# Performance work log

Hardware: AMD Instinct MI355X
Metric: run time of the kernel (lower is better)

## Reference

```python
import jax, jax.numpy as jnp
import numpy as np

KSIZE = 7       # patch size
STRIDE_Q = 4    # stride_1: query patch stride
STRIDE_KV = 1   # stride_2: key/value patch stride
SCALE = 10.0    # softmax_scale


def unfold(x, k, stride, pad):
    """torch.nn.Unfold equivalent. x:[B,C,H,W] -> [B, C*k*k, L] (c-major, then kh, kw)."""
    x = jnp.pad(x, ((0, 0), (0, 0), (pad, pad), (pad, pad)))
    B, C, Hp, Wp = x.shape
    nh = (Hp - k) // stride + 1
    nw = (Wp - k) // stride + 1
    sl = lambda i, n: slice(i, i + (n - 1) * stride + 1, stride)
    # [B, C, k*k, nh, nw]
    pat = jnp.stack([x[:, :, sl(i, nh), sl(j, nw)] for i in range(k) for j in range(k)], axis=2)
    return pat.reshape(B, C * k * k, nh * nw)


def fold(p, k, stride, pad, H, W):
    """torch.nn.functional.fold equivalent (overlap-add). p:[B, C*k*k, L] -> [B,C,H,W]."""
    B, D, L = p.shape
    C = D // (k * k)
    nh = (H + 2 * pad - k) // stride + 1
    nw = (W + 2 * pad - k) // stride + 1
    p = p.reshape(B, C, k, k, nh, nw)
    out = jnp.zeros((B, C, H + 2 * pad, W + 2 * pad), p.dtype)
    sl = lambda i, n: slice(i, i + (n - 1) * stride + 1, stride)
    for i in range(k):
        for j in range(k):
            out = out.at[:, :, sl(i, nh), sl(j, nw)].add(p[:, :, i, j])
    return out[:, :, pad:pad + H, pad:pad + W]


def conv1x1(x, w, bias):
    # w: [out, in]
    return jnp.einsum('bihw,oi->bohw', x, w) + bias[None, :, None, None]


def setup_inputs() -> dict:
    key = jax.random.key(0)
    ks = jax.random.split(key, 9)
    B, Cin, H, W = 4, 64, 128, 128
    Cit = 16
    s_in = 1.0 / np.sqrt(Cin)
    s_it = 1.0 / np.sqrt(Cit)
    return {
        'b': jax.random.normal(ks[0], (B, Cin, H, W), jnp.float32),
        'g_w': jax.random.normal(ks[1], (Cit, Cin), jnp.float32) * s_in,
        'g_b': jax.random.normal(ks[2], (Cit,), jnp.float32) * 0.01,
        'th_w': jax.random.normal(ks[3], (Cit, Cin), jnp.float32) * s_in,
        'th_b': jax.random.normal(ks[4], (Cit,), jnp.float32) * 0.01,
        'ph_w': jax.random.normal(ks[5], (Cit, Cin), jnp.float32) * s_in,
        'ph_b': jax.random.normal(ks[6], (Cit,), jnp.float32) * 0.01,
        'o_w': jax.random.normal(ks[7], (Cin, Cit), jnp.float32) * s_it,
        'o_b': jax.random.normal(ks[8], (Cin,), jnp.float32) * 0.01,
    }


def reference(b, g_w, g_b, th_w, th_b, ph_w, ph_b, o_w, o_b):
    B, Cin, H, W = b.shape
    pad = KSIZE // 2
    b1 = conv1x1(b, g_w, g_b)      # queries source  [B,16,H,W]
    b2 = conv1x1(b, th_w, th_b)    # values source
    b3 = conv1x1(b, ph_w, ph_b)    # keys source

    Q = unfold(b1, KSIZE, STRIDE_Q, pad).transpose(0, 2, 1)   # [B, L1, D]
    K = unfold(b3, KSIZE, STRIDE_KV, pad).transpose(0, 2, 1)  # [B, L2, D]
    V = unfold(b2, KSIZE, STRIDE_KV, pad).transpose(0, 2, 1)  # [B, L2, D]

    scores = jnp.einsum('bqd,bkd->bqk', Q, K)                 # [B, L1, L2]
    attn = jax.nn.softmax(scores * SCALE, axis=-1)
    Zp = jnp.einsum('bqk,bkd->bqd', attn, V).transpose(0, 2, 1)  # [B, D, L1]

    y = fold(Zp, KSIZE, STRIDE_Q, pad, H, W)                  # overlap-add
    Zc = fold(jnp.ones_like(Zp), KSIZE, STRIDE_Q, pad, H, W)  # overlap counts
    y = y / Zc
    y = conv1x1(y, o_w, o_b)
    return b + y
```

## Files before the change

kernel.cpp:

```cpp
#include <hip/hip_runtime.h>
#include <math.h>

#define NB 4
#define CIN 64
#define CIT 16
#define KS 7
#define PAD 3
#define HH 128
#define WW 128
#define HP 134
#define WPS 136
#define L1 1024
#define DD 784
#define SCALE_F 10.0f
#define WSCR 3.5f
#define TCAP 128
#define WEPS 1e-7f

#define NPIX (HP * WPS)
#define NHWCF (NB * NPIX * CIT)
#define RSTR 2176

typedef __attribute__((ext_vector_type(4))) float f32x4;
typedef __attribute__((ext_vector_type(8))) short s16x8;
typedef __attribute__((ext_vector_type(4))) unsigned int u32x4;

__device__ __forceinline__ unsigned short f2bf(float f) {
    unsigned u = __float_as_uint(f);
    unsigned r = (u + 0x7FFFu + ((u >> 16) & 1u)) >> 16;
    return (unsigned short)r;
}

__global__ __launch_bounds__(256) void k_prep(
    const float* __restrict__ bin,
    const float* __restrict__ gw, const float* __restrict__ gb,
    const float* __restrict__ tw, const float* __restrict__ tb,
    const float* __restrict__ pw, const float* __restrict__ pb,
    float* __restrict__ b1f, float* __restrict__ b2f, float* __restrict__ b3f,
    unsigned short* __restrict__ b1n, unsigned short* __restrict__ b3n)
{
    int p = blockIdx.x * 256 + threadIdx.x;
    if (p >= NB * NPIX) return;
    int x = p % WPS; int r = p / WPS; int y = r % HP; int bb = r / HP;
    bool inter = (x >= PAD && x < PAD + WW && y >= PAD && y < PAD + HH);
    float v[CIN];
    if (inter) {
        int iy = y - PAD, ix = x - PAD;
        const float* src = bin + ((size_t)(bb * CIN) * HH + iy) * WW + ix;
        #pragma unroll
        for (int ci = 0; ci < CIN; ++ci) v[ci] = src[ci * HH * WW];
    }
    float a1v[CIT], a2v[CIT], a3v[CIT];
    unsigned short o1[CIT], o3[CIT];
    #pragma unroll
    for (int co = 0; co < CIT; ++co) {
        float a1 = 0.f, a2 = 0.f, a3 = 0.f;
        if (inter) {
            a1 = gb[co]; a2 = tb[co]; a3 = pb[co];
            #pragma unroll
            for (int ci = 0; ci < CIN; ++ci) {
                float vv = v[ci];
                a1 += gw[co * CIN + ci] * vv;
                a2 += tw[co * CIN + ci] * vv;
                a3 += pw[co * CIN + ci] * vv;
            }
        }
        a1v[co] = a1; a2v[co] = a2; a3v[co] = a3;
        o1[co] = f2bf(a1); o3[co] = f2bf(a3);
    }
    size_t pb16 = (size_t)p * CIT;
    #pragma unroll
    for (int g = 0; g < 4; ++g) {
        f32x4 w1 = {a1v[4*g], a1v[4*g+1], a1v[4*g+2], a1v[4*g+3]};
        f32x4 w2 = {a2v[4*g], a2v[4*g+1], a2v[4*g+2], a2v[4*g+3]};
        f32x4 w3 = {a3v[4*g], a3v[4*g+1], a3v[4*g+2], a3v[4*g+3]};
        *(f32x4*)(b1f + pb16 + 4*g) = w1;
        *(f32x4*)(b2f + pb16 + 4*g) = w2;
        *(f32x4*)(b3f + pb16 + 4*g) = w3;
    }
    unsigned pk1[8], pk3[8];
    #pragma unroll
    for (int kk = 0; kk < 8; ++kk) {
        pk1[kk] = (unsigned)o1[2 * kk] | ((unsigned)o1[2 * kk + 1] << 16);
        pk3[kk] = (unsigned)o3[2 * kk] | ((unsigned)o3[2 * kk + 1] << 16);
    }
    unsigned short* d1 = b1n + pb16;
    unsigned short* d3 = b3n + pb16;
    u32x4 w1a = {pk1[0], pk1[1], pk1[2], pk1[3]}, w1b = {pk1[4], pk1[5], pk1[6], pk1[7]};
    u32x4 w3a = {pk3[0], pk3[1], pk3[2], pk3[3]}, w3b = {pk3[4], pk3[5], pk3[6], pk3[7]};
    *(u32x4*)d1 = w1a; *(u32x4*)(d1 + 8) = w1b;
    *(u32x4*)d3 = w3a; *(u32x4*)(d3 + 8) = w3b;
}

__global__ __launch_bounds__(512, 2) void k_screen(
    const unsigned short* __restrict__ b1n, const unsigned short* __restrict__ b3n,
    _Float16* __restrict__ tmaxh)
{
    int blk = blockIdx.x;
    int qt = blk & 3;
    int qh = (blk >> 2) & 31;
    int bb = blk >> 7;
    int qstart_ky = qt * 32;
    int tid = threadIdx.x;
    int lane = tid & 63, w = tid >> 6;
    int lanelow = lane & 15;
    int h = (lane >> 5) & 1;
    int clo = (lane >> 4) & 1;

    __shared__ __align__(16) short smem[16 * RSTR];

    const unsigned short* b1nb = b1n + (size_t)bb * (NPIX * CIT);
    const unsigned short* b3nb = b3n + (size_t)bb * (NPIX * CIT);

    int qybase = 4 * qh;
    size_t qb0 = ((size_t)((bb * 64 + 2 * qh) * 16 + lanelow)) * 1024 + qt * 256 + w;
    size_t qb1 = ((size_t)((bb * 64 + 2 * qh + 1) * 16 + lanelow)) * 1024 + qt * 256 + w;

    for (int task = tid; task < 1600; task += 512) {
        int pp = task % 50, qq = task / 50;
        u32x4 lo = {0, 0, 0, 0}, hi = {0, 0, 0, 0};
        if (pp < 49) {
            int i = pp / 7, j = pp % 7;
            int qx = 4 * qq;
            const unsigned short* src = b1nb + ((size_t)(qybase + i) * WPS + qx + j) * CIT;
            lo = *(const u32x4*)src; hi = *(const u32x4*)(src + 8);
        }
        short* dst = smem + (qq * 50 + pp) * 16;
        *(u32x4*)dst = lo; *(u32x4*)(dst + 8) = hi;
    }
    __syncthreads();

    s16x8 B0[25], B1[25];
    #pragma unroll
    for (int s = 0; s < 25; ++s) {
        int ko = s * 32 + ((lane >> 4) & 3) * 8;
        B0[s] = *(const s16x8*)(smem + lanelow * 800 + ko);
        B1[s] = *(const s16x8*)(smem + (lanelow + 16) * 800 + ko);
    }
    __syncthreads();

    short* kring = smem;
    for (int task = tid; task < 16 * 272; task += 512) {
        int rr = task / 272, ch = task % 272;
        *(u32x4*)(kring + rr * RSTR + ch * 8) =
            *(const u32x4*)(b3nb + (size_t)(qstart_ky + rr) * (WPS * CIT) + ch * 8);
    }
    __syncthreads();

    int abase = (w * 16 + lanelow) * 16 + clo * 8;

    for (int p = 0; p < 4; ++p) {
        __builtin_amdgcn_s_setprio(1);
        for (int it8 = 0; it8 < 8; ++it8) {
            int it = 8 * p + it8;
            int ky = qstart_ky + it;
            f32x4 C0 = {0.f, 0.f, 0.f, 0.f}, C1 = {0.f, 0.f, 0.f, 0.f};
            #pragma unroll
            for (int s = 0; s < 25; ++s) {
                const int pe = 2 * s;
                const int po = (2 * s + 1 < 49) ? (2 * s + 1) : 0;
                const int ie = pe / 7, je = pe % 7;
                const int io = po / 7, jo = po % 7;
                int i_h = h ? io : ie;
                int j_h = h ? jo : je;
                int slot = (ky + i_h) & 15;
                const short* ap = kring + slot * RSTR + j_h * 16 + abase;
                s16x8 a0 = *(const s16x8*)ap;
                C0 = __builtin_amdgcn_mfma_f32_16x16x32_bf16(a0, B0[s], C0, 0, 0, 0);
                C1 = __builtin_amdgcn_mfma_f32_16x16x32_bf16(a0, B1[s], C1, 0, 0, 0);
            }
            float lm0 = fmaxf(fmaxf(C0[0], C0[1]), fmaxf(C0[2], C0[3]));
            lm0 = fmaxf(lm0, __shfl_xor(lm0, 16));
            lm0 = fmaxf(lm0, __shfl_xor(lm0, 32));
            float lm1 = fmaxf(fmaxf(C1[0], C1[1]), fmaxf(C1[2], C1[3]));
            lm1 = fmaxf(lm1, __shfl_xor(lm1, 16));
            lm1 = fmaxf(lm1, __shfl_xor(lm1, 32));
            if (lane < 16) {
                tmaxh[qb0 + it * 8] = (_Float16)lm0;
                tmaxh[qb1 + it * 8] = (_Float16)lm1;
            }
        }
        __builtin_amdgcn_s_setprio(0);
        __syncthreads();
        if (p < 3) {
            int rbase = qstart_ky + 8 * p + 16;
            for (int task = tid; task < 8 * 272; task += 512) {
                int rr = task / 272, ch = task % 272;
                int row = rbase + rr;
                int srow = (row < HP) ? row : (HP - 1);
                *(u32x4*)(kring + (row & 15) * RSTR + ch * 8) =
                    *(const u32x4*)(b3nb + (size_t)srow * (WPS * CIT) + ch * 8);
            }
            __syncthreads();
        }
    }
}

__global__ __launch_bounds__(256) void k_finalize(
    const float* __restrict__ b1f, const float* __restrict__ b2f,
    const float* __restrict__ b3f, const _Float16* __restrict__ tmaxh,
    float* __restrict__ Zp)
{
    int wv = threadIdx.x >> 6;
    int lane = threadIdx.x & 63;
    int gq = blockIdx.x * 4 + wv;
    int bb = gq >> 10, q = gq & 1023;
    int qh = q >> 5, qw = q & 31;
    int qy = qh * 4, qx = qw * 4;
    int ch = lane & 15, pbase = lane >> 4;

    __shared__ int tq[4][TCAP];

    const float* b1b = b1f + (size_t)bb * (NPIX * CIT);
    const float* b2b = b2f + (size_t)bb * (NPIX * CIT);
    const float* b3b = b3f + (size_t)bb * (NPIX * CIT);

    const _Float16* qb = tmaxh + ((size_t)((bb * 64 + (q >> 4)) * 16 + (q & 15))) * 1024;
    _Float16 tvh[16];
    *(u32x4*)&tvh[0] = *(const u32x4*)(qb + (size_t)lane * 16);
    *(u32x4*)&tvh[8] = *(const u32x4*)(qb + (size_t)lane * 16 + 8);
    float tv[16]; float mg = -1e30f;
    #pragma unroll
    for (int k = 0; k < 16; ++k) {
        tv[k] = (float)tvh[k];
        mg = fmaxf(mg, tv[k]);
    }
    #pragma unroll
    for (int o = 32; o > 0; o >>= 1) mg = fmaxf(mg, __shfl_xor(mg, o));
    float thr = mg - WSCR;

    int cnt = 0;
    #pragma unroll
    for (int k = 0; k < 16; ++k) {
        bool p = (tv[k] >= thr);
        unsigned long long mk = __ballot(p);
        if (p) {
            int pos = cnt + (int)__popcll(mk & ((1ull << lane) - 1ull));
            if (pos < TCAP) tq[wv][pos] = lane * 16 + k;
        }
        cnt += (int)__popcll(mk);
    }
    int nt = min(cnt, TCAP);
    int n = nt * 16;
    __syncthreads();

    float qreg[13]; int offs[13];
    int qorg = (qy * WPS + qx) * CIT;
    #pragma unroll
    for (int k = 0; k < 13; ++k) {
        int p = pbase + 4 * k;
        if (p < 49) {
            int pi = p / 7, pj = p % 7;
            offs[k] = (pi * WPS + pj) * CIT + ch;
            qreg[k] = b1b[qorg + offs[k]];
        } else { offs[k] = 0; qreg[k] = 0.f; }
    }

    float m = -1e30f, l = 0.f, acc[13];
    #pragma unroll
    for (int k = 0; k < 13; ++k) acc[k] = 0.f;

    for (int ci0 = 0; ci0 < n; ci0 += 4) {
        int kb[4];
        #pragma unroll
        for (int u = 0; u < 4; ++u) {
            int ci = ci0 + u;
            int e = tq[wv][ci >> 4];
            int ky = (e >> 8) * 32 + ((e >> 3) & 31);
            int kx = (e & 7) * 16 + (ci & 15);
            kb[u] = (ky * WPS + kx) * CIT;
        }
        float kv[4][13];
        #pragma unroll
        for (int u = 0; u < 4; ++u)
            #pragma unroll
            for (int k = 0; k < 13; ++k) kv[u][k] = b3b[kb[u] + offs[k]];
        float s[4];
        #pragma unroll
        for (int u = 0; u < 4; ++u) {
            float t = 0.f;
            #pragma unroll
            for (int k = 0; k < 13; ++k) t += qreg[k] * kv[u][k];
            #pragma unroll
            for (int o = 32; o > 0; o >>= 1) t += __shfl_xor(t, o);
            s[u] = t;
        }
        float mnew = fmaxf(m, fmaxf(fmaxf(s[0], s[1]), fmaxf(s[2], s[3])));
        float sc = __expf(SCALE_F * (m - mnew));
        float w0 = __expf(SCALE_F * (s[0] - mnew));
        float w1 = __expf(SCALE_F * (s[1] - mnew));
        float w2 = __expf(SCALE_F * (s[2] - mnew));
        float w3 = __expf(SCALE_F * (s[3] - mnew));
        l = l * sc + (w0 + w1 + w2 + w3);
        m = mnew;
        float wmx = fmaxf(fmaxf(w0, w1), fmaxf(w2, w3));
        if (wmx > WEPS) {
            float vv[4][13];
            #pragma unroll
            for (int u = 0; u < 4; ++u)
                #pragma unroll
                for (int k = 0; k < 13; ++k) vv[u][k] = b2b[kb[u] + offs[k]];
            #pragma unroll
            for (int k = 0; k < 13; ++k)
                acc[k] = acc[k] * sc + w0 * vv[0][k] + w1 * vv[1][k]
                                     + w2 * vv[2][k] + w3 * vv[3][k];
        }
    }

    float inv = (n > 0) ? (1.f / l) : 0.f;
    float* zq = Zp + (size_t)gq * DD;
    #pragma unroll
    for (int k = 0; k < 13; ++k) {
        int d = lane + 64 * k;
        if (d < DD) zq[d] = acc[k] * inv;
    }
}

__global__ __launch_bounds__(256) void k_fold(
    const float* __restrict__ bin, const float* __restrict__ ow,
    const float* __restrict__ ob, const float* __restrict__ Zp,
    float* __restrict__ outp)
{
    int p = blockIdx.x * 256 + threadIdx.x;
    if (p >= NB * HH * WW) return;
    int ox = p % WW; int r = p / WW; int oy = r % HH; int bb = r / HH;
    int yp = oy + PAD, xp = ox + PAD;
    int qh0 = (yp - 3) >> 2, qh1 = min(31, yp >> 2);
    int qw0 = (xp - 3) >> 2, qw1 = min(31, xp >> 2);
    float cnt = (float)((qh1 - qh0 + 1) * (qw1 - qw0 + 1));
    float y16[CIT];
    #pragma unroll
    for (int c = 0; c < CIT; ++c) y16[c] = 0.f;
    for (int qhh = qh0; qhh <= qh1; ++qhh) {
        int i = yp - 4 * qhh;
        for (int qww = qw0; qww <= qw1; ++qww) {
            int j = xp - 4 * qww;
            const float* zb = Zp + (size_t)((bb << 10) + qhh * 32 + qww) * DD + (i * 7 + j) * CIT;
            #pragma unroll
            for (int c = 0; c < CIT; ++c) y16[c] += zb[c];
        }
    }
    float icnt = 1.f / cnt;
    #pragma unroll
    for (int c = 0; c < CIT; ++c) y16[c] *= icnt;
    size_t oidx = ((size_t)(bb * CIN) * HH + oy) * WW + ox;
    for (int co = 0; co < CIN; ++co) {
        float a = ob[co];
        #pragma unroll
        for (int c = 0; c < CIT; ++c) a += ow[co * CIT + c] * y16[c];
        outp[oidx + (size_t)co * HH * WW] = bin[oidx + (size_t)co * HH * WW] + a;
    }
}

extern "C" void kernel_launch(void* const* d_in, const int* in_sizes, int n_in,
                              void* d_out, int out_size, void* d_ws, size_t ws_size,
                              hipStream_t stream) {
    (void)in_sizes; (void)n_in; (void)out_size; (void)ws_size;
    const float* bin = (const float*)d_in[0];
    const float* gw  = (const float*)d_in[1];
    const float* gb  = (const float*)d_in[2];
    const float* tw  = (const float*)d_in[3];
    const float* tb  = (const float*)d_in[4];
    const float* pw  = (const float*)d_in[5];
    const float* pb  = (const float*)d_in[6];
    const float* ow  = (const float*)d_in[7];
    const float* ob  = (const float*)d_in[8];

    float* outp = (float*)d_out;
    float* b3f = outp;
    float* b1f = outp + NHWCF;
    unsigned short* b3n = (unsigned short*)(outp + 2 * (size_t)NHWCF);
    unsigned short* b1n = b3n + NHWCF;

    float* ws = (float*)d_ws;
    float* b2f = ws;
    float* Zp  = ws + NHWCF;
    _Float16* tmaxh = (_Float16*)(ws + NHWCF + (size_t)NB * L1 * DD);

    hipLaunchKernelGGL(k_prep, dim3((NB * NPIX + 255) / 256), dim3(256), 0, stream,
                       bin, gw, gb, tw, tb, pw, pb, b1f, b2f, b3f, b1n, b3n);
    hipLaunchKernelGGL(k_screen, dim3(512), dim3(512), 0, stream,
                       b1n, b3n, tmaxh);
    hipLaunchKernelGGL(k_finalize, dim3(1024), dim3(256), 0, stream,
                       b1f, b2f, b3f, tmaxh, Zp);
    hipLaunchKernelGGL(k_fold, dim3((NB * HH * WW + 255) / 256), dim3(256), 0, stream,
                       bin, ow, ob, Zp, outp);
}
```

Measured before the change: 241.5 us.

## Stage key window tile in LDS per candidate tile and skip negligible value loads

For each candidate key tile, the wavefront now cooperatively loads the 7-row by 22-pixel key window (16 channels each) into shared memory once. The 16 key candidates then read their 7x7 patches from LDS instead of issuing redundant global gathers. Value accumulation is also gated per key on its softmax weight, so loads are skipped for negligible weights. The cost is about 39 KB of LDS per block, which may reduce occupancy, plus extra fill work when only a few keys in a tile matter.

```diff
diff --git a/kernel.cpp b/kernel.cpp
--- a/kernel.cpp
+++ b/kernel.cpp
@@ -20,6 +20,7 @@
 #define NPIX (HP * WPS)
 #define NHWCF (NB * NPIX * CIT)
 #define RSTR 2176
+#define WROW 352
 
 typedef __attribute__((ext_vector_type(4))) float f32x4;
 typedef __attribute__((ext_vector_type(8))) short s16x8;
@@ -210,6 +211,7 @@
     int ch = lane & 15, pbase = lane >> 4;
 
     __shared__ int tq[4][TCAP];
+    __shared__ __align__(16) float wbufs[4][7 * WROW];
 
     const float* b1b = b1f + (size_t)bb * (NPIX * CIT);
     const float* b2b = b2f + (size_t)bb * (NPIX * CIT);
@@ -241,10 +243,9 @@
         cnt += (int)__popcll(mk);
     }
     int nt = min(cnt, TCAP);
-    int n = nt * 16;
     __syncthreads();
 
-    float qreg[13]; int offs[13];
+    float qreg[13]; int offs[13]; int loff[13];
     int qorg = (qy * WPS + qx) * CIT;
     #pragma unroll
     for (int k = 0; k < 13; ++k) {
@@ -252,62 +253,74 @@
         if (p < 49) {
             int pi = p / 7, pj = p % 7;
             offs[k] = (pi * WPS + pj) * CIT + ch;
+            loff[k] = pi * WROW + pj * CIT + ch;
             qreg[k] = b1b[qorg + offs[k]];
-        } else { offs[k] = 0; qreg[k] = 0.f; }
-    }
+        } else { offs[k] = 0; loff[k] = 0; qreg[k] = 0.f; }
+    }
+    float* wbuf = wbufs[wv];
 
     float m = -1e30f, l = 0.f, acc[13];
     #pragma unroll
     for (int k = 0; k < 13; ++k) acc[k] = 0.f;
 
-    for (int ci0 = 0; ci0 < n; ci0 += 4) {
-        int kb[4];
+    for (int ti = 0; ti < nt; ++ti) {
+        int e = tq[wv][ti];
+        int ky = e >> 3;
+        int kxb = (e & 7) * 16;
+        const float* wsrc = b3b + (size_t)(ky * WPS + kxb) * CIT;
         #pragma unroll
-        for (int u = 0; u < 4; ++u) {
-            int ci = ci0 + u;
-            int e = tq[wv][ci >> 4];
-            int ky = (e >> 8) * 32 + ((e >> 3) & 31);
-            int kx = (e & 7) * 16 + (ci & 15);
-            kb[u] = (ky * WPS + kx) * CIT;
-        }
-        float kv[4][13];
-        #pragma unroll
-        for (int u = 0; u < 4; ++u)
+        for (int t = 0; t < 10; ++t) {
+            int task = lane + 64 * t;
+            if (task < 616) {
+                int row = task / 88, xf = (task % 88) * 4;
+                *(f32x4*)(wbuf + row * WROW + xf) =
+                    *(const f32x4*)(wsrc + (size_t)row * (WPS * CIT) + xf);
+            }
+        }
+        for (int c4 = 0; c4 < 4; ++c4) {
+            float kvv[4][13];
             #pragma unroll
-            for (int k = 0; k < 13; ++k) kv[u][k] = b3b[kb[u] + offs[k]];
-        float s[4];
-        #pragma unroll
-        for (int u = 0; u < 4; ++u) {
-            float t = 0.f;
+            for (int u = 0; u < 4; ++u) {
+                int cib = (c4 * 4 + u) * CIT;
+                #pragma unroll
+                for (int k = 0; k < 13; ++k) kvv[u][k] = wbuf[loff[k] + cib];
+            }
+            float s[4];
             #pragma unroll
-            for (int k = 0; k < 13; ++k) t += qreg[k] * kv[u][k];
-            #pragma unroll
-            for (int o = 32; o > 0; o >>= 1) t += __shfl_xor(t, o);
-            s[u] = t;
-        }
-        float mnew = fmaxf(m, fmaxf(fmaxf(s[0], s[1]), fmaxf(s[2], s[3])));
-        float sc = __expf(SCALE_F * (m - mnew));
-        float w0 = __expf(SCALE_F * (s[0] - mnew));
-        float w1 = __expf(SCALE_F * (s[1] - mnew));
-        float w2 = __expf(SCALE_F * (s[2] - mnew));
-        float w3 = __expf(SCALE_F * (s[3] - mnew));
-        l = l * sc + (w0 + w1 + w2 + w3);
-        m = mnew;
-        float wmx = fmaxf(fmaxf(w0, w1), fmaxf(w2, w3));
-        if (wmx > WEPS) {
-            float vv[4][13];
-            #pragma unroll
-            for (int u = 0; u < 4; ++u)
+            for (int u = 0; u < 4; ++u) {
+                float t = 0.f;
                 #pragma unroll
-                for (int k = 0; k < 13; ++k) vv[u][k] = b2b[kb[u] + offs[k]];
-            #pragma unroll
-            for (int k = 0; k < 13; ++k)
-                acc[k] = acc[k] * sc + w0 * vv[0][k] + w1 * vv[1][k]
-                                     + w2 * vv[2][k] + w3 * vv[3][k];
-        }
-    }
-
-    float inv = (n > 0) ? (1.f / l) : 0.f;
+                for (int k = 0; k < 13; ++k) t += qreg[k] * kvv[u][k];
+                #pragma unroll
+                for (int o = 32; o > 0; o >>= 1) t += __shfl_xor(t, o);
+                s[u] = t;
+            }
+            float mnew = fmaxf(m, fmaxf(fmaxf(s[0], s[1]), fmaxf(s[2], s[3])));
+            float sc = __expf(SCALE_F * (m - mnew));
+            float wk[4];
+            wk[0] = __expf(SCALE_F * (s[0] - mnew));
+            wk[1] = __expf(SCALE_F * (s[1] - mnew));
+            wk[2] = __expf(SCALE_F * (s[2] - mnew));
+            wk[3] = __expf(SCALE_F * (s[3] - mnew));
+            l = l * sc + (wk[0] + wk[1] + wk[2] + wk[3]);
+            m = mnew;
+            float wmx = fmaxf(fmaxf(wk[0], wk[1]), fmaxf(wk[2], wk[3]));
+            if (wmx > WEPS) {
+                #pragma unroll
+                for (int k = 0; k < 13; ++k) acc[k] *= sc;
+                #pragma unroll
+                for (int u = 0; u < 4; ++u) {
+                    if (wk[u] > WEPS) {
+                        int kb = (ky * WPS + kxb + c4 * 4 + u) * CIT;
+                        #pragma unroll
+                        for (int k = 0; k < 13; ++k) acc[k] += wk[u] * b2b[kb + offs[k]];
+                    }
+                }
+            }
+        }
+    }
+
+    float inv = (nt > 0) ? (1.f / l) : 0.f;
     float* zq = Zp + (size_t)gq * DD;
     #pragma unroll
     for (int k = 0; k < 13; ++k) {
```

Result: faster. 215.5 us (-10.8%).
